# Optimization experiments

Hardware: AMD Instinct MI355X
Metric: run time of the kernel (lower is better)

The kernel has to match this reference:

```python
import jax, jax.numpy as jnp
import numpy as np

# ---- dims ----
N_NODES = 33      # nodes per graph (33-bus grid)
SEQ     = 24      # time steps per sample
BATCH   = 64      # samples
G       = BATCH * SEQ          # total graphs in the batch
EPG     = 64                   # directed edges per graph
E       = G * EPG              # total edges
N       = G * N_NODES          # total nodes
IN_CH   = 2
HID     = 64
HEADS   = 8
HC      = HID * HEADS          # 512
EDGE_DIM = 3
LSTM1_H = 128
LSTM2_H = 64
N_CLASSES = 4
NEG_SLOPE = 0.2


def setup_inputs() -> dict:
    key = jax.random.key(0)
    ks = jax.random.split(key, 32)
    rng = np.random.default_rng(0)

    # block-structured edge_index: every edge stays inside its own graph
    off = np.repeat(np.arange(G, dtype=np.int64) * N_NODES, EPG)
    src = rng.integers(0, N_NODES, E) + off
    dst = rng.integers(0, N_NODES, E) + off
    edge_index = jnp.asarray(np.stack([src, dst]), dtype=jnp.int32)

    def glorot(k, shape):
        fan = shape[0] + shape[-1]
        s = jnp.sqrt(6.0 / fan).astype(jnp.float32)
        return jax.random.uniform(k, shape, jnp.float32, -s, s)

    inp = dict(
        x=jax.random.normal(ks[0], (N, IN_CH), jnp.float32),
        edge_index=edge_index,
        edge_attr=jax.random.uniform(ks[1], (E, EDGE_DIM), jnp.float32),
        # GATv2 layer 1 (concat=True)
        g1_Wl=glorot(ks[2], (IN_CH, HC)),
        g1_Wr=glorot(ks[3], (IN_CH, HC)),
        g1_We=glorot(ks[4], (EDGE_DIM, HC)),
        g1_att=glorot(ks[5], (HEADS, HID)),
        g1_b=jnp.zeros((HC,), jnp.float32),
        # GATv2 layer 2 (concat=False -> head mean)
        g2_Wl=glorot(ks[6], (HC, HC)),
        g2_Wr=glorot(ks[7], (HC, HC)),
        g2_We=glorot(ks[8], (EDGE_DIM, HC)),
        g2_att=glorot(ks[9], (HEADS, HID)),
        g2_b=jnp.zeros((HID,), jnp.float32),
        # LSTM1: input 33*64=2112 -> 128, gates ordered (i,f,g,o)
        l1_Wih=0.05 * jax.random.normal(ks[10], (4 * LSTM1_H, N_NODES * HID), jnp.float32),
        l1_Whh=0.05 * jax.random.normal(ks[11], (4 * LSTM1_H, LSTM1_H), jnp.float32),
        l1_bih=jnp.zeros((4 * LSTM1_H,), jnp.float32),
        l1_bhh=jnp.zeros((4 * LSTM1_H,), jnp.float32),
        # LSTM2: 128 -> 64
        l2_Wih=0.05 * jax.random.normal(ks[12], (4 * LSTM2_H, LSTM1_H), jnp.float32),
        l2_Whh=0.05 * jax.random.normal(ks[13], (4 * LSTM2_H, LSTM2_H), jnp.float32),
        l2_bih=jnp.zeros((4 * LSTM2_H,), jnp.float32),
        l2_bhh=jnp.zeros((4 * LSTM2_H,), jnp.float32),
        # FC 64 -> n_classes
        fc_W=0.05 * jax.random.normal(ks[14], (N_CLASSES, LSTM2_H), jnp.float32),
        fc_b=jnp.zeros((N_CLASSES,), jnp.float32),
    )
    return inp


def _gatv2(x, edge_attr, src, dst, Wl, Wr, We, att, b, concat):
    """PyG GATv2Conv with edge_dim, add_self_loops semantics omitted is NOT used:
    we follow the message math: m = leaky_relu(xl[src]+xr[dst]+We@e),
    alpha = segment_softmax(<m,att>, dst), out = scatter_add(alpha * xl[src])."""
    n = x.shape[0]
    xl = (x @ Wl).reshape(n, HEADS, HID)      # [N,H,C]
    xr = (x @ Wr).reshape(n, HEADS, HID)
    em = (edge_attr @ We).reshape(-1, HEADS, HID)  # [E,H,C]
    m = jax.nn.leaky_relu(xl[src] + xr[dst] + em, NEG_SLOPE)
    logits = jnp.einsum('ehc,hc->eh', m, att)          # [E,H]
    mx = jax.ops.segment_max(logits, dst, num_segments=n)   # [N,H]
    ex = jnp.exp(logits - mx[dst])
    den = jax.ops.segment_sum(ex, dst, num_segments=n)
    alpha = ex / (den[dst] + 1e-16)                    # [E,H]
    out = jax.ops.segment_sum(xl[src] * alpha[:, :, None], dst, num_segments=n)  # [N,H,C]
    out = out.reshape(n, HC) if concat else out.mean(axis=1)
    return out + b


def _lstm(x, Wih, Whh, bih, bhh, hsz):
    B = x.shape[0]
    h0 = jnp.zeros((B, hsz), x.dtype)
    c0 = jnp.zeros((B, hsz), x.dtype)

    def step(carry, xt):
        h, c = carry
        gates = xt @ Wih.T + h @ Whh.T + bih + bhh
        i, f, g, o = jnp.split(gates, 4, axis=-1)
        i = jax.nn.sigmoid(i); f = jax.nn.sigmoid(f)
        g = jnp.tanh(g);       o = jax.nn.sigmoid(o)
        c = f * c + i * g
        h = o * jnp.tanh(c)
        return (h, c), h

    _, ys = jax.lax.scan(step, (h0, c0), x.transpose(1, 0, 2))  # [T,B,H]
    return ys.transpose(1, 0, 2)


def reference(x, edge_index, edge_attr,
              g1_Wl, g1_Wr, g1_We, g1_att, g1_b,
              g2_Wl, g2_Wr, g2_We, g2_att, g2_b,
              l1_Wih, l1_Whh, l1_bih, l1_bhh,
              l2_Wih, l2_Whh, l2_bih, l2_bhh,
              fc_W, fc_b):
    src, dst = edge_index[0], edge_index[1]
    h = jax.nn.elu(_gatv2(x, edge_attr, src, dst, g1_Wl, g1_Wr, g1_We, g1_att, g1_b, True))
    h = jax.nn.elu(_gatv2(h, edge_attr, src, dst, g2_Wl, g2_Wr, g2_We, g2_att, g2_b, False))
    seq = h.reshape(BATCH, SEQ, N_NODES * HID)          # [B,T,2112]
    seq = _lstm(seq, l1_Wih, l1_Whh, l1_bih, l1_bhh, LSTM1_H)
    seq = _lstm(seq, l2_Wih, l2_Whh, l2_bih, l2_bhh, LSTM2_H)
    last = seq[:, -1, :]                                 # [B,64]
    return last @ fc_W.T + fc_b                          # [B,n_classes]
```

## Files before the change

kernel.cpp:

```cpp
#include <hip/hip_runtime.h>
#include <math.h>

#define N_NODES 33
#define SEQ 24
#define BATCH 64
#define G_GRAPHS (BATCH * SEQ)
#define EPG 64
#define E_EDGES (G_GRAPHS * EPG)
#define N_TOTAL (G_GRAPHS * N_NODES)
#define HID 64
#define HEADS 8
#define HC (HID * HEADS)
#define LSTM1_H 128
#define LSTM2_H 64
#define NEG_SLOPE 0.2f
#define CONV_BLOCKS (2048 + (512 * 2112 + 255) / 256)

__device__ __forceinline__ float sigmoidf_(float x) { return 1.f / (1.f + expf(-x)); }
__device__ __forceinline__ float eluf_(float x) { return x > 0.f ? x : expm1f(x); }
__device__ __forceinline__ float lreluf_(float x) { return x > 0.f ? x : NEG_SLOPE * x; }

typedef __attribute__((ext_vector_type(4))) float f32x4;
typedef _Float16 half_t;
typedef __attribute__((ext_vector_type(8))) _Float16 halfx8;

__device__ __forceinline__ void gl2lds16(const void* g, void* l) {
  __builtin_amdgcn_global_load_lds(
      (__attribute__((address_space(1))) const unsigned int*)g,
      (__attribute__((address_space(3))) unsigned int*)l, 16, 0, 0);
}

__global__ __launch_bounds__(256) void gat1_kernel(
    const float* __restrict__ x, const int* __restrict__ src, const int* __restrict__ dst,
    const float* __restrict__ ea, const float* __restrict__ Wl, const float* __restrict__ Wr,
    const float* __restrict__ We, const float* __restrict__ att, const float* __restrict__ bias,
    half_t* __restrict__ h1, int g0, int gat_blocks,
    const float* __restrict__ g2Wl, const float* __restrict__ g2Wr,
    half_t* __restrict__ B2, const float* __restrict__ W1, half_t* __restrict__ W1f) {
  const int tid = threadIdx.x;
  if ((int)blockIdx.x >= gat_blocks) {
    int cb = blockIdx.x - gat_blocks;
    if (cb < 2048) {
      int idx = cb * 256 + tid;
      int n = idx >> 9, k = idx & 511;
      float v = (n < 512) ? g2Wl[k * 512 + n] : g2Wr[k * 512 + (n - 512)];
      B2[idx] = (half_t)v;
    } else {
      int idx = (cb - 2048) * 256 + tid;
      if (idx < 512 * 2112) W1f[idx] = (half_t)W1[idx];
    }
    return;
  }

  __shared__ alignas(16) float Wl_s[2 * 512];
  __shared__ alignas(16) float Wr_s[2 * 512];
  __shared__ alignas(16) float We_s[3 * 512];
  __shared__ alignas(16) float att_s[512];
  __shared__ float xs0_s[N_NODES + 1], xs1_s[N_NODES + 1];
  __shared__ float easX[EPG], easY[EPG], easZ[EPG];
  __shared__ float logit_s[HEADS * 65];
  __shared__ int sloc[EPG], dloc[EPG], deg[N_NODES], start[N_NODES], fill[N_NODES], elist[EPG];

  const int g = g0 + blockIdx.x;
  const int nb = g * N_NODES, eb = g * EPG;
  const int lb = blockIdx.x * N_NODES;

  for (int i = tid; i < 1024; i += 256) { Wl_s[i] = Wl[i]; Wr_s[i] = Wr[i]; }
  for (int i = tid; i < 1536; i += 256) We_s[i] = We[i];
  for (int i = tid; i < 512; i += 256) att_s[i] = att[i];
  if (tid < 2 * N_NODES) {
    float v = x[nb * 2 + tid];
    if (tid & 1) xs1_s[tid >> 1] = v; else xs0_s[tid >> 1] = v;
  }
  if (tid < EPG) {
    easX[tid] = ea[(eb + tid) * 3 + 0];
    easY[tid] = ea[(eb + tid) * 3 + 1];
    easZ[tid] = ea[(eb + tid) * 3 + 2];
    sloc[tid] = src[eb + tid] - nb;
    dloc[tid] = dst[eb + tid] - nb;
  }
  if (tid < N_NODES) { deg[tid] = 0; fill[tid] = 0; }
  __syncthreads();
  if (tid < EPG) atomicAdd(&deg[dloc[tid]], 1);
  __syncthreads();
  if (tid == 0) { int a = 0; for (int n = 0; n < N_NODES; ++n) { start[n] = a; a += deg[n]; } }
  __syncthreads();
  if (tid < EPG) { int d = dloc[tid]; int p = atomicAdd(&fill[d], 1); elist[start[d] + p] = tid; }

  for (int t = tid; t < EPG * HEADS; t += 256) {
    int h = t >> 6, e = t & 63;
    int s = sloc[e], d = dloc[e];
    float xs0 = xs0_s[s], xs1 = xs1_s[s], xd0 = xs0_s[d], xd1 = xs1_s[d];
    float e0 = easX[e], e1 = easY[e], e2 = easZ[e];
    float acc = 0.f;
    int base = h * 64;
    #pragma unroll
    for (int c4 = 0; c4 < 16; ++c4) {
      int j = base + c4 * 4;
      f32x4 wl0 = *(const f32x4*)(Wl_s + j);
      f32x4 wl1 = *(const f32x4*)(Wl_s + 512 + j);
      f32x4 wr0 = *(const f32x4*)(Wr_s + j);
      f32x4 wr1 = *(const f32x4*)(Wr_s + 512 + j);
      f32x4 we0 = *(const f32x4*)(We_s + j);
      f32x4 we1 = *(const f32x4*)(We_s + 512 + j);
      f32x4 we2 = *(const f32x4*)(We_s + 1024 + j);
      f32x4 at  = *(const f32x4*)(att_s + j);
      #pragma unroll
      for (int q = 0; q < 4; ++q) {
        float v = xs0 * wl0[q] + xs1 * wl1[q]
                + xd0 * wr0[q] + xd1 * wr1[q]
                + e0 * we0[q] + e1 * we1[q] + e2 * we2[q];
        acc += lreluf_(v) * at[q];
      }
    }
    logit_s[h * 65 + e] = acc;
  }
  __syncthreads();

  for (int t = tid; t < HEADS * 64; t += 256) {
    int h = t >> 6, n = t & 63;
    if (n < N_NODES) {
      int s0 = start[n], dn = deg[n];
      float mx = -1e30f;
      for (int i = 0; i < dn; ++i) mx = fmaxf(mx, logit_s[h * 65 + elist[s0 + i]]);
      float den = 0.f;
      for (int i = 0; i < dn; ++i) den += expf(logit_s[h * 65 + elist[s0 + i]] - mx);
      float inv = 1.f / (den + 1e-16f);
      for (int i = 0; i < dn; ++i) {
        int e = elist[s0 + i];
        logit_s[h * 65 + e] = expf(logit_s[h * 65 + e] - mx) * inv;
      }
    }
  }
  __syncthreads();

  for (int t = tid; t < N_NODES * 64; t += 256) {
    int n = t >> 6, jb = t & 63;
    int j0 = jb * 8, h = jb >> 3;
    f32x4 wa0 = *(const f32x4*)(Wl_s + j0);
    f32x4 wa1 = *(const f32x4*)(Wl_s + j0 + 4);
    f32x4 wb0 = *(const f32x4*)(Wl_s + 512 + j0);
    f32x4 wb1 = *(const f32x4*)(Wl_s + 512 + j0 + 4);
    float acc[8] = {};
    int s0 = start[n], dn = deg[n];
    for (int i = 0; i < dn; ++i) {
      int e = elist[s0 + i]; int s = sloc[e];
      float a = logit_s[h * 65 + e];
      float ax0 = a * xs0_s[s], ax1 = a * xs1_s[s];
      #pragma unroll
      for (int q = 0; q < 4; ++q) {
        acc[q]     += ax0 * wa0[q] + ax1 * wb0[q];
        acc[4 + q] += ax0 * wa1[q] + ax1 * wb1[q];
      }
    }
    f32x4 b0 = *(const f32x4*)(bias + j0);
    f32x4 b1 = *(const f32x4*)(bias + j0 + 4);
    halfx8 vh;
    #pragma unroll
    for (int cc = 0; cc < 8; ++cc) {
      float bb = (cc < 4) ? b0[cc] : b1[cc - 4];
      vh[cc] = (half_t)eluf_(acc[cc] + bb);
    }
    *(halfx8*)(h1 + (size_t)(lb + n) * HC + j0) = vh;
  }
}

template <int WM, int WN, int NP, int K, int SA, int SB, typename TC>
__global__ __launch_bounds__(256) void gemm_f16(
    const half_t* __restrict__ A, const half_t* __restrict__ B,
    TC* __restrict__ C, const float* __restrict__ bias1, const float* __restrict__ bias2,
    int M, int N) {
  constexpr int BM = 32 * WM, BN = 32 * WN;
  constexpr bool BOUNCE = (sizeof(TC) == 2) && (BM == 128) && (BN == 128);
  constexpr int STAGE_HALFS = (BM + BN) * 32 * NP;
  constexpr int CT_HALFS = BOUNCE ? 128 * 132 : 0;
  constexpr int LDS_HALFS = STAGE_HALFS > CT_HALFS ? STAGE_HALFS : CT_HALFS;
  __shared__ half_t lds[LDS_HALFS];
  half_t* A_s = lds;
  half_t* B_s = A_s + NP * BM * 32;

  const int R = M / BM, NT = N / BN;
  int b = blockIdx.x;
  int xcd = b & 7, q = b >> 3;
  int ct = q % NT, rg = q / NT;
  int r = rg * 8 + xcd;
  if (r >= R) return;

  const int tid = threadIdx.x;
  const int wave = tid >> 6, lane = tid & 63;
  const int wm = wave >> 1, wn = wave & 1;
  const int bm = r * BM, bn = ct * BN;

  const int rA = lane >> 2;
  const int swz = (rA & 3) ^ ((rA >> 2) & 3);
  const int cA = ((lane & 3) ^ swz) * 8;

  f32x4 acc[WM][WN];
  #pragma unroll
  for (int tm = 0; tm < WM; ++tm)
    #pragma unroll
    for (int tn = 0; tn < WN; ++tn) acc[tm][tn] = {0.f, 0.f, 0.f, 0.f};

  for (int k0 = 0; k0 < K; k0 += 32 * NP) {
    #pragma unroll
    for (int p = 0; p < NP; ++p) {
      int kk = k0 + p * 32;
      #pragma unroll
      for (int i = 0; i < BM / 64; ++i) {
        int row = i * 64 + wave * 16;
        gl2lds16(A + (size_t)(bm + row + rA) * SA + kk + cA,
                 A_s + p * BM * 32 + row * 32);
      }
      #pragma unroll
      for (int i = 0; i < BN / 64; ++i) {
        int row = i * 64 + wave * 16;
        gl2lds16(B + (size_t)(bn + row + rA) * SB + kk + cA,
                 B_s + p * BN * 32 + row * 32);
      }
    }
    __syncthreads();

    const int fr = lane & 15;
    const int fs = (fr & 3) ^ ((fr >> 2) & 3);
    const int fk = ((lane >> 4) ^ fs) * 8;
    #pragma unroll
    for (int p = 0; p < NP; ++p) {
      const int pA = p * BM * 32, pB = p * BN * 32;
      halfx8 af[WM], bf[WN];
      #pragma unroll
      for (int tm = 0; tm < WM; ++tm) {
        int rr = (wm * WM + tm) * 16 + fr;
        af[tm] = *(const halfx8*)(A_s + pA + rr * 32 + fk);
      }
      #pragma unroll
      for (int tn = 0; tn < WN; ++tn) {
        int rr = (wn * WN + tn) * 16 + fr;
        bf[tn] = *(const halfx8*)(B_s + pB + rr * 32 + fk);
      }
      #pragma unroll
      for (int tm = 0; tm < WM; ++tm)
        #pragma unroll
        for (int tn = 0; tn < WN; ++tn)
          acc[tm][tn] = __builtin_amdgcn_mfma_f32_16x16x32_f16(af[tm], bf[tn], acc[tm][tn], 0, 0, 0);
    }
    __syncthreads();
  }

  const int col0 = lane & 15, rq = (lane >> 4) * 4;
  if constexpr (BOUNCE) {
    half_t* Cs = lds;
    #pragma unroll
    for (int tm = 0; tm < WM; ++tm)
      #pragma unroll
      for (int tn = 0; tn < WN; ++tn) {
        int cl = (wn * WN + tn) * 16 + col0;
        #pragma unroll
        for (int rr = 0; rr < 4; ++rr) {
          int rl = (wm * WM + tm) * 16 + rq + rr;
          Cs[rl * 132 + cl] = (half_t)acc[tm][tn][rr];
        }
      }
    __syncthreads();
    #pragma unroll
    for (int pass = 0; pass < 8; ++pass) {
      int row = pass * 16 + (tid >> 4);
      int col = (tid & 15) * 8;
      halfx8 v = *(const halfx8*)(Cs + row * 132 + col);
      *(halfx8*)((half_t*)C + (size_t)(bm + row) * N + bn + col) = v;
    }
  } else {
    #pragma unroll
    for (int tm = 0; tm < WM; ++tm)
      #pragma unroll
      for (int tn = 0; tn < WN; ++tn) {
        int col = bn + (wn * WN + tn) * 16 + col0;
        float badd = 0.f;
        if (bias1) badd += bias1[col];
        if (bias2) badd += bias2[col];
        #pragma unroll
        for (int rr = 0; rr < 4; ++rr) {
          int row = bm + (wm * WM + tm) * 16 + rq + rr;
          C[(size_t)row * N + col] = (TC)(acc[tm][tn][rr] + badd);
        }
      }
  }
}

__global__ __launch_bounds__(256) void gemm_f16_splitk(
    const half_t* __restrict__ A, const half_t* __restrict__ B,
    float* __restrict__ Cp, const float* __restrict__ bias1, const float* __restrict__ bias2,
    int M, int N) {
  constexpr int SA = 2112;
  __shared__ half_t lds[(64 + 64) * 64];
  half_t* A_s = lds;
  half_t* B_s = A_s + 2 * 64 * 32;

  const int part = blockIdx.y;
  const int koff = part ? 576 + (part - 1) * 512 : 0;
  const int kend = part ? 512 : 576;
  const half_t* Ap = A + koff;
  const half_t* Bp = B + koff;
  float* C = Cp + (size_t)part * M * N;

  const int R = M / 64, NT = N / 64;
  int b = blockIdx.x;
  int xcd = b & 7, q = b >> 3;
  int ct = q % NT, rg = q / NT;
  int r = rg * 8 + xcd;
  if (r >= R) return;

  const int tid = threadIdx.x;
  const int wave = tid >> 6, lane = tid & 63;
  const int wm = wave >> 1, wn = wave & 1;
  const int bm = r * 64, bn = ct * 64;

  const int rA = lane >> 2;
  const int swz = (rA & 3) ^ ((rA >> 2) & 3);
  const int cA = ((lane & 3) ^ swz) * 8;

  f32x4 acc[2][2];
  #pragma unroll
  for (int tm = 0; tm < 2; ++tm)
    #pragma unroll
    for (int tn = 0; tn < 2; ++tn) acc[tm][tn] = {0.f, 0.f, 0.f, 0.f};

  for (int k0 = 0; k0 < kend; k0 += 64) {
    #pragma unroll
    for (int p = 0; p < 2; ++p) {
      int kk = k0 + p * 32;
      {
        int row = wave * 16;
        gl2lds16(Ap + (size_t)(bm + row + rA) * SA + kk + cA,
                 A_s + p * 64 * 32 + row * 32);
        gl2lds16(Bp + (size_t)(bn + row + rA) * SA + kk + cA,
                 B_s + p * 64 * 32 + row * 32);
      }
    }
    __syncthreads();
    const int fr = lane & 15;
    const int fs = (fr & 3) ^ ((fr >> 2) & 3);
    const int fk = ((lane >> 4) ^ fs) * 8;
    #pragma unroll
    for (int p = 0; p < 2; ++p) {
      const int pA = p * 64 * 32, pB = p * 64 * 32;
      halfx8 af[2], bf[2];
      #pragma unroll
      for (int tm = 0; tm < 2; ++tm) {
        int rr = (wm * 2 + tm) * 16 + fr;
        af[tm] = *(const halfx8*)(A_s + pA + rr * 32 + fk);
      }
      #pragma unroll
      for (int tn = 0; tn < 2; ++tn) {
        int rr = (wn * 2 + tn) * 16 + fr;
        bf[tn] = *(const halfx8*)(B_s + pB + rr * 32 + fk);
      }
      #pragma unroll
      for (int tm = 0; tm < 2; ++tm)
        #pragma unroll
        for (int tn = 0; tn < 2; ++tn)
          acc[tm][tn] = __builtin_amdgcn_mfma_f32_16x16x32_f16(af[tm], bf[tn], acc[tm][tn], 0, 0, 0);
    }
    __syncthreads();
  }

  const int col0 = lane & 15, rq = (lane >> 4) * 4;
  #pragma unroll
  for (int tm = 0; tm < 2; ++tm)
    #pragma unroll
    for (int tn = 0; tn < 2; ++tn) {
      int col = bn + (wn * 2 + tn) * 16 + col0;
      float badd = (part == 0) ? (bias1[col] + bias2[col]) : 0.f;
      #pragma unroll
      for (int rr = 0; rr < 2 * 2; ++rr) { }
      #pragma unroll
      for (int rr = 0; rr < 4; ++rr) {
        int row = bm + (wm * 2 + tm) * 16 + rq + rr;
        C[(size_t)row * N + col] = acc[tm][tn][rr] + badd;
      }
    }
}

__global__ __launch_bounds__(256) void gat2_kernel(
    const half_t* __restrict__ xlr, const int* __restrict__ src, const int* __restrict__ dst,
    const float* __restrict__ ea, const float* __restrict__ We,
    const float* __restrict__ att, const float* __restrict__ bias,
    half_t* __restrict__ h2, int g0) {
  __shared__ alignas(16) float We_s[3 * 512];
  __shared__ alignas(16) float att_s[512];
  __shared__ float b_s[HID];
  __shared__ float easX[EPG], easY[EPG], easZ[EPG];
  __shared__ float logit_s[HEADS * 65];
  __shared__ int sloc[EPG], dloc[EPG], deg[N_NODES], start[N_NODES], fill[N_NODES], elist[EPG];

  const int g = g0 + blockIdx.x, tid = threadIdx.x;
  const int nb = g * N_NODES, eb = g * EPG;
  const int lb = blockIdx.x * N_NODES;
  const int wave = tid >> 6, lane = tid & 63;

  for (int i = tid; i < 1536; i += 256) We_s[i] = We[i];
  for (int i = tid; i < 512; i += 256) att_s[i] = att[i];
  if (tid < HID) b_s[tid] = bias[tid];
  if (tid < EPG) {
    easX[tid] = ea[(eb + tid) * 3 + 0];
    easY[tid] = ea[(eb + tid) * 3 + 1];
    easZ[tid] = ea[(eb + tid) * 3 + 2];
    sloc[tid] = src[eb + tid] - nb;
    dloc[tid] = dst[eb + tid] - nb;
  }
  if (tid < N_NODES) { deg[tid] = 0; fill[tid] = 0; }
  __syncthreads();
  if (tid < EPG) atomicAdd(&deg[dloc[tid]], 1);
  __syncthreads();
  if (tid == 0) { int a = 0; for (int n = 0; n < N_NODES; ++n) { start[n] = a; a += deg[n]; } }
  __syncthreads();
  if (tid < EPG) { int d = dloc[tid]; int p = atomicAdd(&fill[d], 1); elist[start[d] + p] = tid; }
  __syncthreads();

  const int j0 = lane * 8;
  float w0[8], w1[8], w2[8], at8[8];
  #pragma unroll
  for (int q = 0; q < 8; ++q) {
    w0[q] = We_s[j0 + q];
    w1[q] = We_s[512 + j0 + q];
    w2[q] = We_s[1024 + j0 + q];
    at8[q] = att_s[j0 + q];
  }

  for (int e = wave; e < EPG; e += 4) {
    int s = sloc[e], d = dloc[e];
    halfx8 xlv = *((const halfx8*)(xlr + (size_t)(lb + s) * 1024) + lane);
    halfx8 xrv = *((const halfx8*)(xlr + (size_t)(lb + d) * 1024 + 512) + lane);
    float e0 = easX[e], e1 = easY[e], e2 = easZ[e];
    float acc = 0.f;
    #pragma unroll
    for (int q = 0; q < 8; ++q) {
      float v = (float)xlv[q] + (float)xrv[q] + e0 * w0[q] + e1 * w1[q] + e2 * w2[q];
      acc += lreluf_(v) * at8[q];
    }
    acc += __shfl_xor(acc, 1, 64);
    acc += __shfl_xor(acc, 2, 64);
    acc += __shfl_xor(acc, 4, 64);
    if ((lane & 7) == 0) logit_s[(lane >> 3) * 65 + e] = acc;
  }
  __syncthreads();

  for (int t = tid; t < HEADS * 64; t += 256) {
    int h = t >> 6, n = t & 63;
    if (n < N_NODES) {
      int s0 = start[n], dn = deg[n];
      float mx = -1e30f;
      for (int i = 0; i < dn; ++i) mx = fmaxf(mx, logit_s[h * 65 + elist[s0 + i]]);
      float den = 0.f;
      for (int i = 0; i < dn; ++i) den += expf(logit_s[h * 65 + elist[s0 + i]] - mx);
      float inv = 1.f / (den + 1e-16f);
      for (int i = 0; i < dn; ++i) {
        int e = elist[s0 + i];
        logit_s[h * 65 + e] = expf(logit_s[h * 65 + e] - mx) * inv;
      }
    }
  }
  __syncthreads();

  for (int n = wave; n < N_NODES; n += 4) {
    float acc = 0.f;
    int s0 = start[n], dn = deg[n];
    for (int i = 0; i < dn; ++i) {
      int e = elist[s0 + i], s = sloc[e];
      const half_t* row = xlr + (size_t)(lb + s) * 1024 + lane;
      #pragma unroll
      for (int h = 0; h < 8; ++h)
        acc += logit_s[h * 65 + e] * (float)row[h * 64];
    }
    float v = eluf_(acc * 0.125f + b_s[lane]);
    h2[(size_t)(nb + n) * HID + lane] = (half_t)v;
  }
}

__global__ __launch_bounds__(1024, 4) void lstm_all(
    const float* __restrict__ X0, const float* __restrict__ X1,
    const float* __restrict__ X2p, const float* __restrict__ X3,
    const float* __restrict__ Whh1,
    const float* __restrict__ Wih2, const float* __restrict__ bih2,
    const float* __restrict__ bhh2, const float* __restrict__ Whh2,
    const float* __restrict__ fcW, const float* __restrict__ fcb,
    float* __restrict__ out) {
  __shared__ float hs1[LSTM1_H], cs1[LSTM1_H], p1[512], gs1[512];
  __shared__ float Y1s[SEQ][LSTM1_H];
  __shared__ float hs2[LSTM2_H], cs2[LSTM2_H], p2[4 * 256], gs2[256];
  const int tid = threadIdx.x, b = blockIdx.x;
  const int j = tid & 511, half = tid >> 9;

  float4 w1[16];
  {
    const float4* wp = (const float4*)(Whh1 + (size_t)j * LSTM1_H + half * 64);
    #pragma unroll
    for (int q = 0; q < 16; ++q) w1[q] = wp[q];
  }
  if (tid < LSTM1_H) { hs1[tid] = 0.f; cs1[tid] = 0.f; }
  __syncthreads();
  for (int t = 0; t < SEQ; ++t) {
    const float* hb = hs1 + half * 64;
    float acc = 0.f;
    #pragma unroll
    for (int q = 0; q < 16; ++q) {
      acc += w1[q].x * hb[4 * q] + w1[q].y * hb[4 * q + 1]
           + w1[q].z * hb[4 * q + 2] + w1[q].w * hb[4 * q + 3];
    }
    if (half) p1[j] = acc;
    __syncthreads();
    if (!half) {
      size_t xo = ((size_t)b * SEQ + t) * 512 + j;
      gs1[j] = acc + p1[j] + X0[xo] + X1[xo] + X2p[xo] + X3[xo];
    }
    __syncthreads();
    if (tid < LSTM1_H) {
      float ig = sigmoidf_(gs1[tid]);
      float fg = sigmoidf_(gs1[LSTM1_H + tid]);
      float gg = tanhf(gs1[2 * LSTM1_H + tid]);
      float og = sigmoidf_(gs1[3 * LSTM1_H + tid]);
      float c = fg * cs1[tid] + ig * gg;
      cs1[tid] = c;
      float h = og * tanhf(c);
      hs1[tid] = h;
      Y1s[t][tid] = h;
    }
    __syncthreads();
  }

  const int j2 = tid & 255, qt = tid >> 8;
  float4 w2x[8], w2h[4];
  {
    const float4* wxp = (const float4*)(Wih2 + (size_t)j2 * LSTM1_H + qt * 32);
    #pragma unroll
    for (int q = 0; q < 8; ++q) w2x[q] = wxp[q];
    const float4* whp = (const float4*)(Whh2 + (size_t)j2 * LSTM2_H + qt * 16);
    #pragma unroll
    for (int q = 0; q < 4; ++q) w2h[q] = whp[q];
  }
  if (tid < LSTM2_H) { hs2[tid] = 0.f; cs2[tid] = 0.f; }
  __syncthreads();
  for (int t = 0; t < SEQ; ++t) {
    const float* y = Y1s[t] + qt * 32;
    const float* hb = hs2 + qt * 16;
    float acc = 0.f;
    #pragma unroll
    for (int q = 0; q < 8; ++q) {
      acc += w2x[q].x * y[4 * q] + w2x[q].y * y[4 * q + 1]
           + w2x[q].z * y[4 * q + 2] + w2x[q].w * y[4 * q + 3];
    }
    #pragma unroll
    for (int q = 0; q < 4; ++q) {
      acc += w2h[q].x * hb[4 * q] + w2h[q].y * hb[4 * q + 1]
           + w2h[q].z * hb[4 * q + 2] + w2h[q].w * hb[4 * q + 3];
    }
    p2[qt * 256 + j2] = acc;
    __syncthreads();
    if (qt == 0)
      gs2[j2] = p2[j2] + p2[256 + j2] + p2[512 + j2] + p2[768 + j2]
              + bih2[j2] + bhh2[j2];
    __syncthreads();
    if (tid < LSTM2_H) {
      float ig = sigmoidf_(gs2[tid]);
      float fg = sigmoidf_(gs2[LSTM2_H + tid]);
      float gg = tanhf(gs2[2 * LSTM2_H + tid]);
      float og = sigmoidf_(gs2[3 * LSTM2_H + tid]);
      float c = fg * cs2[tid] + ig * gg;
      cs2[tid] = c;
      hs2[tid] = og * tanhf(c);
    }
    __syncthreads();
  }
  if (tid < 4) {
    float acc = fcb[tid];
    #pragma unroll
    for (int k = 0; k < LSTM2_H; ++k) acc += fcW[tid * LSTM2_H + k] * hs2[k];
    out[b * 4 + tid] = acc;
  }
}

extern "C" void kernel_launch(void* const* d_in, const int* in_sizes, int n_in,
                              void* d_out, int out_size, void* d_ws, size_t ws_size,
                              hipStream_t stream) {
  const float* x       = (const float*)d_in[0];
  const int*   eidx    = (const int*)d_in[1];
  const float* eattr   = (const float*)d_in[2];
  const float* g1_Wl   = (const float*)d_in[3];
  const float* g1_Wr   = (const float*)d_in[4];
  const float* g1_We   = (const float*)d_in[5];
  const float* g1_att  = (const float*)d_in[6];
  const float* g1_b    = (const float*)d_in[7];
  const float* g2_Wl   = (const float*)d_in[8];
  const float* g2_Wr   = (const float*)d_in[9];
  const float* g2_We   = (const float*)d_in[10];
  const float* g2_att  = (const float*)d_in[11];
  const float* g2_b    = (const float*)d_in[12];
  const float* l1_Wih  = (const float*)d_in[13];
  const float* l1_Whh  = (const float*)d_in[14];
  const float* l1_bih  = (const float*)d_in[15];
  const float* l1_bhh  = (const float*)d_in[16];
  const float* l2_Wih  = (const float*)d_in[17];
  const float* l2_Whh  = (const float*)d_in[18];
  const float* l2_bih  = (const float*)d_in[19];
  const float* l2_bhh  = (const float*)d_in[20];
  const float* fc_W    = (const float*)d_in[21];
  const float* fc_b    = (const float*)d_in[22];
  float* out = (float*)d_out;

  const int* src = eidx;
  const int* dst = eidx + E_EDGES;

  const int cand[5] = {1, 2, 3, 4, 6};
  int nchunks = 0;
  half_t *h1 = nullptr, *xlr2c = nullptr, *h2 = nullptr, *B2 = nullptr, *W1f = nullptr;
  float *X1p = nullptr;
  int chunk_g = 0, chunk_n = 0;
  for (int ci = 0; ci < 5; ++ci) {
    int C = cand[ci];
    int CG = G_GRAPHS / C, CN = CG * N_NODES;
    char* p = (char*)d_ws;
    auto alloc = [&](size_t bytes) { char* r = p; p += (bytes + 255) & ~(size_t)255; return r; };
    half_t* t_h1    = (half_t*)alloc((size_t)CN * HC * 2);
    half_t* t_xlr2c = (half_t*)alloc((size_t)CN * 1024 * 2);
    half_t* t_h2    = (half_t*)alloc((size_t)G_GRAPHS * 2112 * 2);
    half_t* t_B2    = (half_t*)alloc((size_t)1024 * 512 * 2);
    half_t* t_W1f   = (half_t*)alloc((size_t)512 * 2112 * 2);
    float*  t_X1p   = (float*)alloc((size_t)4 * G_GRAPHS * 512 * 4);
    if ((size_t)(p - (char*)d_ws) <= ws_size) {
      nchunks = C; chunk_g = CG; chunk_n = CN;
      h1 = t_h1; xlr2c = t_xlr2c; h2 = t_h2; B2 = t_B2; W1f = t_W1f;
      X1p = t_X1p;
      break;
    }
  }
  if (nchunks == 0) return;

  for (int c = 0; c < nchunks; ++c) {
    int g0 = c * chunk_g;
    int extra = (c == 0) ? CONV_BLOCKS : 0;
    gat1_kernel<<<chunk_g + extra, 256, 0, stream>>>(
        x, src, dst, eattr, g1_Wl, g1_Wr, g1_We, g1_att, g1_b, h1, g0, chunk_g,
        g2_Wl, g2_Wr, B2, l1_Wih, W1f);
    int R = chunk_n / 128, NT = 1024 / 128;
    int gblocks = 8 * ((R + 7) / 8) * NT;
    gemm_f16<4, 4, 2, HC, HC, HC, half_t><<<gblocks, 256, 0, stream>>>(
        h1, B2, xlr2c, (const float*)nullptr, (const float*)nullptr,
        chunk_n, 1024);
    gat2_kernel<<<chunk_g, 256, 0, stream>>>(xlr2c, src, dst, eattr, g2_We,
                                             g2_att, g2_b, h2, g0);
  }

  {
    dim3 grid(192, 4);
    gemm_f16_splitk<<<grid, 256, 0, stream>>>(h2, W1f, X1p, l1_bih, l1_bhh,
                                              G_GRAPHS, 512);
  }

  {
    size_t PS = (size_t)G_GRAPHS * 512;
    lstm_all<<<BATCH, 1024, 0, stream>>>(X1p, X1p + PS, X1p + 2 * PS, X1p + 3 * PS,
                                         l1_Whh, l2_Wih, l2_bih, l2_bhh, l2_Whh,
                                         fc_W, fc_b, out);
  }
}
```

Measured before the change: 355.8 us.

## Use 512-thread GAT blocks and tiled LDS transpose for weight conversion

Doubles the block size of both GAT kernels so each thread handles one (head, edge) or (head, node) pair and gat2 spreads edges and nodes across eight waves. The weight-conversion side blocks now transpose g2_Wl/g2_Wr through a padded LDS tile for coalesced reads and writes, and convert W1 with eight elements per thread, cutting the extra block count sharply. This adds a 16KB LDS tile to every gat1 block, which may lower occupancy, and larger blocks can raise register pressure.

```diff
diff --git a/kernel.cpp b/kernel.cpp
--- a/kernel.cpp
+++ b/kernel.cpp
@@ -14,7 +14,7 @@
 #define LSTM1_H 128
 #define LSTM2_H 64
 #define NEG_SLOPE 0.2f
-#define CONV_BLOCKS (2048 + (512 * 2112 + 255) / 256)
+#define CONV_BLOCKS (128 + 264)
 
 __device__ __forceinline__ float sigmoidf_(float x) { return 1.f / (1.f + expf(-x)); }
 __device__ __forceinline__ float eluf_(float x) { return x > 0.f ? x : expm1f(x); }
@@ -30,7 +30,7 @@
       (__attribute__((address_space(3))) unsigned int*)l, 16, 0, 0);
 }
 
-__global__ __launch_bounds__(256) void gat1_kernel(
+__global__ __launch_bounds__(512) void gat1_kernel(
     const float* __restrict__ x, const int* __restrict__ src, const int* __restrict__ dst,
     const float* __restrict__ ea, const float* __restrict__ Wl, const float* __restrict__ Wr,
     const float* __restrict__ We, const float* __restrict__ att, const float* __restrict__ bias,
@@ -38,19 +38,6 @@
     const float* __restrict__ g2Wl, const float* __restrict__ g2Wr,
     half_t* __restrict__ B2, const float* __restrict__ W1, half_t* __restrict__ W1f) {
   const int tid = threadIdx.x;
-  if ((int)blockIdx.x >= gat_blocks) {
-    int cb = blockIdx.x - gat_blocks;
-    if (cb < 2048) {
-      int idx = cb * 256 + tid;
-      int n = idx >> 9, k = idx & 511;
-      float v = (n < 512) ? g2Wl[k * 512 + n] : g2Wr[k * 512 + (n - 512)];
-      B2[idx] = (half_t)v;
-    } else {
-      int idx = (cb - 2048) * 256 + tid;
-      if (idx < 512 * 2112) W1f[idx] = (half_t)W1[idx];
-    }
-    return;
-  }
 
   __shared__ alignas(16) float Wl_s[2 * 512];
   __shared__ alignas(16) float Wr_s[2 * 512];
@@ -60,14 +47,46 @@
   __shared__ float easX[EPG], easY[EPG], easZ[EPG];
   __shared__ float logit_s[HEADS * 65];
   __shared__ int sloc[EPG], dloc[EPG], deg[N_NODES], start[N_NODES], fill[N_NODES], elist[EPG];
+  __shared__ float tr[64 * 65];
+
+  if ((int)blockIdx.x >= gat_blocks) {
+    int cb = blockIdx.x - gat_blocks;
+    if (cb < 128) {
+      int kt = cb & 7, nt = cb >> 3;
+      int k0 = kt * 64, n0 = nt * 64;
+      int r = tid >> 6, c = tid & 63;
+      #pragma unroll
+      for (int rr = 0; rr < 8; ++rr) {
+        int kl = rr * 8 + r;
+        int n = n0 + c;
+        float v = (n < 512) ? g2Wl[(size_t)(k0 + kl) * 512 + n]
+                            : g2Wr[(size_t)(k0 + kl) * 512 + n - 512];
+        tr[kl * 65 + c] = v;
+      }
+      __syncthreads();
+      #pragma unroll
+      for (int rr = 0; rr < 8; ++rr) {
+        int nl = rr * 8 + r;
+        B2[(size_t)(n0 + nl) * 512 + k0 + c] = (half_t)tr[c * 65 + nl];
+      }
+    } else {
+      int base = (cb - 128) * 4096 + tid;
+      #pragma unroll
+      for (int i = 0; i < 8; ++i) {
+        int idx = base + i * 512;
+        if (idx < 512 * 2112) W1f[idx] = (half_t)W1[idx];
+      }
+    }
+    return;
+  }
 
   const int g = g0 + blockIdx.x;
   const int nb = g * N_NODES, eb = g * EPG;
   const int lb = blockIdx.x * N_NODES;
 
-  for (int i = tid; i < 1024; i += 256) { Wl_s[i] = Wl[i]; Wr_s[i] = Wr[i]; }
-  for (int i = tid; i < 1536; i += 256) We_s[i] = We[i];
-  for (int i = tid; i < 512; i += 256) att_s[i] = att[i];
+  for (int i = tid; i < 1024; i += 512) { Wl_s[i] = Wl[i]; Wr_s[i] = Wr[i]; }
+  for (int i = tid; i < 1536; i += 512) We_s[i] = We[i];
+  if (tid < 512) att_s[tid] = att[tid];
   if (tid < 2 * N_NODES) {
     float v = x[nb * 2 + tid];
     if (tid & 1) xs1_s[tid >> 1] = v; else xs0_s[tid >> 1] = v;
@@ -87,8 +106,8 @@
   __syncthreads();
   if (tid < EPG) { int d = dloc[tid]; int p = atomicAdd(&fill[d], 1); elist[start[d] + p] = tid; }
 
-  for (int t = tid; t < EPG * HEADS; t += 256) {
-    int h = t >> 6, e = t & 63;
+  {
+    int h = tid >> 6, e = tid & 63;
     int s = sloc[e], d = dloc[e];
     float xs0 = xs0_s[s], xs1 = xs1_s[s], xd0 = xs0_s[d], xd1 = xs1_s[d];
     float e0 = easX[e], e1 = easY[e], e2 = easZ[e];
@@ -117,8 +136,8 @@
   }
   __syncthreads();
 
-  for (int t = tid; t < HEADS * 64; t += 256) {
-    int h = t >> 6, n = t & 63;
+  {
+    int h = tid >> 6, n = tid & 63;
     if (n < N_NODES) {
       int s0 = start[n], dn = deg[n];
       float mx = -1e30f;
@@ -134,7 +153,7 @@
   }
   __syncthreads();
 
-  for (int t = tid; t < N_NODES * 64; t += 256) {
+  for (int t = tid; t < N_NODES * 64; t += 512) {
     int n = t >> 6, jb = t & 63;
     int j0 = jb * 8, h = jb >> 3;
     f32x4 wa0 = *(const f32x4*)(Wl_s + j0);
@@ -328,13 +347,11 @@
     #pragma unroll
     for (int p = 0; p < 2; ++p) {
       int kk = k0 + p * 32;
-      {
-        int row = wave * 16;
-        gl2lds16(Ap + (size_t)(bm + row + rA) * SA + kk + cA,
-                 A_s + p * 64 * 32 + row * 32);
-        gl2lds16(Bp + (size_t)(bn + row + rA) * SA + kk + cA,
-                 B_s + p * 64 * 32 + row * 32);
-      }
+      int row = wave * 16;
+      gl2lds16(Ap + (size_t)(bm + row + rA) * SA + kk + cA,
+               A_s + p * 64 * 32 + row * 32);
+      gl2lds16(Bp + (size_t)(bn + row + rA) * SA + kk + cA,
+               B_s + p * 64 * 32 + row * 32);
     }
     __syncthreads();
     const int fr = lane & 15;
@@ -371,8 +388,6 @@
       int col = bn + (wn * 2 + tn) * 16 + col0;
       float badd = (part == 0) ? (bias1[col] + bias2[col]) : 0.f;
       #pragma unroll
-      for (int rr = 0; rr < 2 * 2; ++rr) { }
-      #pragma unroll
       for (int rr = 0; rr < 4; ++rr) {
         int row = bm + (wm * 2 + tm) * 16 + rq + rr;
         C[(size_t)row * N + col] = acc[tm][tn][rr] + badd;
@@ -380,7 +395,7 @@
     }
 }
 
-__global__ __launch_bounds__(256) void gat2_kernel(
+__global__ __launch_bounds__(512) void gat2_kernel(
     const half_t* __restrict__ xlr, const int* __restrict__ src, const int* __restrict__ dst,
     const float* __restrict__ ea, const float* __restrict__ We,
     const float* __restrict__ att, const float* __restrict__ bias,
@@ -397,8 +412,8 @@
   const int lb = blockIdx.x * N_NODES;
   const int wave = tid >> 6, lane = tid & 63;
 
-  for (int i = tid; i < 1536; i += 256) We_s[i] = We[i];
-  for (int i = tid; i < 512; i += 256) att_s[i] = att[i];
+  for (int i = tid; i < 1536; i += 512) We_s[i] = We[i];
+  if (tid < 512) att_s[tid] = att[tid];
   if (tid < HID) b_s[tid] = bias[tid];
   if (tid < EPG) {
     easX[tid] = ea[(eb + tid) * 3 + 0];
@@ -426,7 +441,7 @@
     at8[q] = att_s[j0 + q];
   }
 
-  for (int e = wave; e < EPG; e += 4) {
+  for (int e = wave; e < EPG; e += 8) {
     int s = sloc[e], d = dloc[e];
     halfx8 xlv = *((const halfx8*)(xlr + (size_t)(lb + s) * 1024) + lane);
     halfx8 xrv = *((const halfx8*)(xlr + (size_t)(lb + d) * 1024 + 512) + lane);
@@ -444,8 +459,8 @@
   }
   __syncthreads();
 
-  for (int t = tid; t < HEADS * 64; t += 256) {
-    int h = t >> 6, n = t & 63;
+  {
+    int h = tid >> 6, n = tid & 63;
     if (n < N_NODES) {
       int s0 = start[n], dn = deg[n];
       float mx = -1e30f;
@@ -461,7 +476,7 @@
   }
   __syncthreads();
 
-  for (int n = wave; n < N_NODES; n += 4) {
+  for (int n = wave; n < N_NODES; n += 8) {
     float acc = 0.f;
     int s0 = start[n], dn = deg[n];
     for (int i = 0; i < dn; ++i) {
@@ -637,7 +652,7 @@
   for (int c = 0; c < nchunks; ++c) {
     int g0 = c * chunk_g;
     int extra = (c == 0) ? CONV_BLOCKS : 0;
-    gat1_kernel<<<chunk_g + extra, 256, 0, stream>>>(
+    gat1_kernel<<<chunk_g + extra, 512, 0, stream>>>(
         x, src, dst, eattr, g1_Wl, g1_Wr, g1_We, g1_att, g1_b, h1, g0, chunk_g,
         g2_Wl, g2_Wr, B2, l1_Wih, W1f);
     int R = chunk_n / 128, NT = 1024 / 128;
@@ -645,7 +660,7 @@
     gemm_f16<4, 4, 2, HC, HC, HC, half_t><<<gblocks, 256, 0, stream>>>(
         h1, B2, xlr2c, (const float*)nullptr, (const float*)nullptr,
         chunk_n, 1024);
-    gat2_kernel<<<chunk_g, 256, 0, stream>>>(xlr2c, src, dst, eattr, g2_We,
+    gat2_kernel<<<chunk_g, 512, 0, stream>>>(xlr2c, src, dst, eattr, g2_We,
                                              g2_att, g2_b, h2, g0);
   }
 
```

Measured after the change: 344.7 us. 1.03x faster.
